# Optimization experiments

Hardware: AMD Instinct MI355X
Metric: run time of the kernel (lower is better)

## Reference

```python
import jax, jax.numpy as jnp
import numpy as np

B, W, K = 8, 200, 100   # batch, window_size, n_features
KS = 7                   # conv kernel size
HID = 150                # GRU hidden dim
ALPHA = 0.2              # leaky relu slope
FE = 2 * W               # feature GAT embed dim (gatv2 doubles window_size)
TE = 2 * K               # temporal GAT embed dim (gatv2 doubles n_features)


def setup_inputs() -> dict:
    key = jax.random.key(0)
    ks = jax.random.split(key, 16)
    s = lambda k, shape, sc=0.05: jax.random.normal(k, shape, jnp.float32) * sc
    return {
        "x": jax.random.normal(ks[0], (B, W, K), jnp.float32),
        "conv_w": s(ks[1], (K, K, KS)),
        "conv_b": s(ks[2], (K,)),
        "f_lin_w": s(ks[3], (2 * W, FE)),
        "f_lin_b": s(ks[4], (FE,)),
        "f_a": s(ks[5], (FE,)),
        "f_bias": s(ks[6], (K, K)),
        "t_lin_w": s(ks[7], (2 * K, TE)),
        "t_lin_b": s(ks[8], (TE,)),
        "t_a": s(ks[9], (TE,)),
        "t_bias": s(ks[10], (W, W)),
        "w_ih": s(ks[11], (3 * HID, 3 * K)),
        "w_hh": s(ks[12], (3 * HID, HID)),
        "b_ih": s(ks[13], (3 * HID,)),
        "b_hh": s(ks[14], (3 * HID,)),
    }


def _leaky(x):
    return jnp.where(x >= 0, x, ALPHA * x)


def _gatv2(v, lin_w, lin_b, a, bias):
    """GATv2 layer over fully-connected graph. v: (b, N, D).
    e_ij = a . leakyrelu(W [v_i || v_j] + b_lin); out = sigmoid(softmax(e+bias) @ v).
    Splitting W rows avoids materializing the (b,N,N,2D) concat tensor."""
    D = v.shape[-1]
    w1, w2 = lin_w[:D], lin_w[D:]
    si = jnp.einsum('bnd,de->bne', v, w1)  # contribution of node i (repeated)
    sj = jnp.einsum('bnd,de->bne', v, w2)  # contribution of node j (alternating)
    g = _leaky(si[:, :, None, :] + sj[:, None, :, :] + lin_b)  # (b,N,N,E)
    e = jnp.einsum('bije,e->bij', g, a) + bias                 # (b,N,N)
    attn = jax.nn.softmax(e, axis=2)
    return jax.nn.sigmoid(jnp.einsum('bij,bjd->bid', attn, v))  # (b,N,D)


def _forward(x, conv_w, conv_b, f_lin_w, f_lin_b, f_a, f_bias,
             t_lin_w, t_lin_b, t_a, t_bias, w_ih, w_hh, b_ih, b_hh):
    # ConvLayer: permute to (b,K,W), pad 3 both sides, conv1d k=7, relu, permute back
    xc = jnp.transpose(x, (0, 2, 1))
    xc = jax.lax.conv_general_dilated(xc, conv_w, (1,), [((KS - 1) // 2, (KS - 1) // 2)],
                                      dimension_numbers=('NCH', 'OIH', 'NCH'))
    xc = jax.nn.relu(xc + conv_b[None, :, None])
    xc = jnp.transpose(xc, (0, 2, 1))  # (b, W, K)

    # Feature GAT: nodes = features, per-node vector = window
    h_feat = _gatv2(jnp.transpose(xc, (0, 2, 1)), f_lin_w, f_lin_b, f_a, f_bias)
    h_feat = jnp.transpose(h_feat, (0, 2, 1))  # (b, W, K)
    # Temporal GAT: nodes = timesteps, per-node vector = features
    h_temp = _gatv2(xc, t_lin_w, t_lin_b, t_a, t_bias)  # (b, W, K)

    h_cat = jnp.concatenate([xc, h_feat, h_temp], axis=2)  # (b, W, 3K)

    # Single-layer GRU, torch gate order (r, z, n), batch_first; return final hidden
    def step(h, xt):
        gi = xt @ w_ih.T + b_ih
        gh = h @ w_hh.T + b_hh
        ir, iz, inn = jnp.split(gi, 3, axis=-1)
        hr, hz, hn = jnp.split(gh, 3, axis=-1)
        r = jax.nn.sigmoid(ir + hr)
        z = jax.nn.sigmoid(iz + hz)
        n = jnp.tanh(inn + r * hn)
        return (1.0 - z) * n + z * h, None

    h0 = jnp.zeros((x.shape[0], HID), x.dtype)
    h_end, _ = jax.lax.scan(step, h0, jnp.transpose(h_cat, (1, 0, 2)))
    return h_end  # (b, HID)


def reference(x, conv_w, conv_b, f_lin_w, f_lin_b, f_a, f_bias,
              t_lin_w, t_lin_b, t_a, t_bias, w_ih, w_hh, b_ih, b_hh):
    return _forward(x, conv_w, conv_b, f_lin_w, f_lin_b, f_a, f_bias,
                    t_lin_w, t_lin_b, t_a, t_bias, w_ih, w_hh, b_ih, b_hh)
```

## Files before the change

### kernel.cpp

```cpp
#include <hip/hip_runtime.h>
#include <math.h>

#define NB   8
#define NW   200
#define NK   100
#define KSZ  7
#define NHID 150
#define NFE  400
#define NTE  200
#define NG   450
#define NCIN 300
#define ALPHAC 0.2f

typedef __attribute__((ext_vector_type(8))) short bf8;
typedef __attribute__((ext_vector_type(4))) float f32x4;

__device__ __forceinline__ float sigmoidf_(float x){
  return 1.0f/(1.0f + __expf(-x));
}
__device__ __forceinline__ float tanhf_(float x){
  float xc = fminf(fmaxf(x, -15.f), 15.f);
  float e = __expf(2.f*xc);
  return (e - 1.f)/(e + 1.f);
}
__device__ __forceinline__ unsigned short f2bf(float f){
  unsigned int u = __float_as_uint(f);
  unsigned int r = u + 0x7FFFu + ((u>>16)&1u);
  return (unsigned short)(r>>16);
}
__device__ __forceinline__ float lrelu_(float x){
  return fmaxf(x, 0.f) + ALPHAC*fminf(x, 0.f);
}

__global__ void prep_kernel(const float* conv_w, const float* w_ih, const float* w_hh,
                            float* conv_wT, float* w_ihT, unsigned int* Bfrag){
  int idx = blockIdx.x*256 + threadIdx.x;
  const int n1 = NK*NK*KSZ;
  const int n2 = NG*NCIN;
  const int n3 = 32*5*64*4;
  if (idx < n1){
    int k = idx % NK; int it = idx / NK;
    int i = it / KSZ, t = it % KSZ;
    conv_wT[idx] = conv_w[(k*NK + i)*KSZ + t];
  } else if (idx < n1 + n2){
    int o = idx - n1; int g = o % NG; int c = o / NG;
    w_ihT[o] = w_ih[g*NCIN + c];
  } else if (idx < n1 + n2 + n3){
    int o = idx - n1 - n2;
    int n   = o / 1280;
    int rem = o % 1280;
    int ks  = rem / 256;
    int rem2= rem % 256;
    int l   = rem2 >> 2;
    int d   = rem2 & 3;
    int col = n*16 + (l & 15);
    int k0  = ks*32 + (l >> 4)*8 + d*2;
    unsigned short lo = 0, hi = 0;
    if (col < NG){
      if (k0     < NHID) lo = f2bf(w_hh[col*NHID + k0]);
      if (k0 + 1 < NHID) hi = f2bf(w_hh[col*NHID + k0 + 1]);
    }
    Bfrag[o] = ((unsigned int)hi << 16) | lo;
  }
}

__global__ void conv_kernel(const float* x, const float* conv_b, const float* conv_wT, float* xc){
  int idx = blockIdx.x*256 + threadIdx.x;
  if (idx >= NB*NW*NK) return;
  int k = idx % NK; int w = (idx/NK) % NW; int b = idx/(NK*NW);
  float acc = conv_b[k];
  const float* xb = x + b*NW*NK;
  for (int t = 0; t < KSZ; ++t){
    int ws = w + t - 3;
    if (ws < 0 || ws >= NW) continue;
    const float* xr = xb + ws*NK;
    const float* wr = conv_wT + t*NK + k;
    #pragma unroll 4
    for (int i = 0; i < NK; ++i){
      acc += xr[i] * wr[i*KSZ*NK];
    }
  }
  xc[idx] = fmaxf(acc, 0.0f);
}

__global__ void fgat_sisj(const float* xc, const float* f_lin_w, float* si, float* sj){
  __shared__ __align__(16) float vt[NW*4];
  int b = blockIdx.x / 25; int n0 = (blockIdx.x % 25)*4;
  int tid = threadIdx.x;
  for (int d = tid; d < NW; d += 512){
    float4 v = *(const float4*)&xc[(b*NW + d)*NK + n0];
    *(float4*)&vt[d*4] = v;
  }
  __syncthreads();
  if (tid >= NFE) return;
  int e = tid;
  float a1[4] = {0,0,0,0}, a2[4] = {0,0,0,0};
  for (int d = 0; d < NW; ++d){
    float w1 = f_lin_w[d*NFE + e];
    float w2 = f_lin_w[(NW + d)*NFE + e];
    float4 v = *(const float4*)&vt[d*4];
    a1[0] += v.x*w1; a1[1] += v.y*w1; a1[2] += v.z*w1; a1[3] += v.w*w1;
    a2[0] += v.x*w2; a2[1] += v.y*w2; a2[2] += v.z*w2; a2[3] += v.w*w2;
  }
  #pragma unroll
  for (int nn = 0; nn < 4; ++nn){
    si[(b*NK + n0+nn)*NFE + e] = a1[nn];
    sj[(b*NK + n0+nn)*NFE + e] = a2[nn];
  }
}

__global__ void tgat_sisj(const float* xc, const float* t_lin_w, float* si, float* sj){
  __shared__ __align__(16) float vt[NK*4];
  int b = blockIdx.x / 50; int n0 = (blockIdx.x % 50)*4;
  int tid = threadIdx.x;
  for (int idx = tid; idx < 4*25; idx += 256){
    int nn = idx & 3; int d4 = idx >> 2;
    float4 v = *(const float4*)&xc[(b*NW + n0+nn)*NK + d4*4];
    vt[(d4*4+0)*4 + nn] = v.x;
    vt[(d4*4+1)*4 + nn] = v.y;
    vt[(d4*4+2)*4 + nn] = v.z;
    vt[(d4*4+3)*4 + nn] = v.w;
  }
  __syncthreads();
  if (tid >= NTE) return;
  int e = tid;
  float a1[4] = {0,0,0,0}, a2[4] = {0,0,0,0};
  for (int d = 0; d < NK; ++d){
    float w1 = t_lin_w[d*NTE + e];
    float w2 = t_lin_w[(NK + d)*NTE + e];
    float4 v = *(const float4*)&vt[d*4];
    a1[0] += v.x*w1; a1[1] += v.y*w1; a1[2] += v.z*w1; a1[3] += v.w*w1;
    a2[0] += v.x*w2; a2[1] += v.y*w2; a2[2] += v.z*w2; a2[3] += v.w*w2;
  }
  #pragma unroll
  for (int nn = 0; nn < 4; ++nn){
    si[(b*NW + n0+nn)*NTE + e] = a1[nn];
    sj[(b*NW + n0+nn)*NTE + e] = a2[nn];
  }
}

__global__ void fgat_attn(const float* xc, const float* si, const float* sj,
                          const float* f_lin_b, const float* f_a, const float* f_bias,
                          float* h_featT){
  __shared__ __align__(16) float sib[NFE];
  __shared__ __align__(16) float av[NFE];
  __shared__ __align__(16) float attn[NK];
  __shared__ float red[128];
  int b = blockIdx.x / NK, i = blockIdx.x % NK;
  int tid = threadIdx.x;
  {
    const float4* si4 = (const float4*)(si + (b*NK + i)*NFE);
    const float4* lb4 = (const float4*)f_lin_b;
    const float4* fa4 = (const float4*)f_a;
    for (int e4 = tid; e4 < NFE/4; e4 += 128){
      float4 s = si4[e4], l = lb4[e4];
      float4 o; o.x=s.x+l.x; o.y=s.y+l.y; o.z=s.z+l.z; o.w=s.w+l.w;
      *(float4*)&sib[e4*4] = o;
      *(float4*)&av[e4*4]  = fa4[e4];
    }
  }
  __syncthreads();
  float ej = -1e30f;
  if (tid < NK){
    const float4* sjr4 = (const float4*)(sj + (b*NK + tid)*NFE);
    const float4* sib4 = (const float4*)sib;
    const float4* av4  = (const float4*)av;
    float acc = 0.f;
    #pragma unroll 4
    for (int e4 = 0; e4 < NFE/4; ++e4){
      float4 s = sjr4[e4], t = sib4[e4], a = av4[e4];
      acc += a.x*lrelu_(t.x+s.x) + a.y*lrelu_(t.y+s.y)
           + a.z*lrelu_(t.z+s.z) + a.w*lrelu_(t.w+s.w);
    }
    ej = acc + f_bias[i*NK + tid];
  }
  red[tid] = ej; __syncthreads();
  for (int s = 64; s > 0; s >>= 1){ if (tid < s) red[tid] = fmaxf(red[tid], red[tid+s]); __syncthreads(); }
  float m = red[0]; __syncthreads();
  float ex = (tid < NK) ? __expf(ej - m) : 0.f;
  red[tid] = ex; __syncthreads();
  for (int s = 64; s > 0; s >>= 1){ if (tid < s) red[tid] += red[tid+s]; __syncthreads(); }
  float denom = red[0];
  if (tid < NK) attn[tid] = ex / denom;
  __syncthreads();
  for (int d = tid; d < NW; d += 128){
    const float4* xr4 = (const float4*)(xc + (b*NW + d)*NK);
    const float4* at4 = (const float4*)attn;
    float acc = 0.f;
    #pragma unroll 5
    for (int j4 = 0; j4 < NK/4; ++j4){
      float4 v = xr4[j4], a = at4[j4];
      acc += a.x*v.x + a.y*v.y + a.z*v.z + a.w*v.w;
    }
    h_featT[(b*NW + d)*NK + i] = sigmoidf_(acc);
  }
}

__global__ void tgat_attn(const float* xc, const float* si, const float* sj,
                          const float* t_lin_b, const float* t_a, const float* t_bias,
                          float* h_temp){
  __shared__ __align__(16) float sib[NTE];
  __shared__ __align__(16) float av[NTE];
  __shared__ __align__(16) float attn[NW];
  __shared__ float red[256];
  int b = blockIdx.x / NW, i = blockIdx.x % NW;
  int tid = threadIdx.x;
  {
    const float4* si4 = (const float4*)(si + (b*NW + i)*NTE);
    const float4* lb4 = (const float4*)t_lin_b;
    const float4* ta4 = (const float4*)t_a;
    for (int e4 = tid; e4 < NTE/4; e4 += 256){
      float4 s = si4[e4], l = lb4[e4];
      float4 o; o.x=s.x+l.x; o.y=s.y+l.y; o.z=s.z+l.z; o.w=s.w+l.w;
      *(float4*)&sib[e4*4] = o;
      *(float4*)&av[e4*4]  = ta4[e4];
    }
  }
  __syncthreads();
  float ej = -1e30f;
  if (tid < NW){
    const float4* sjr4 = (const float4*)(sj + (b*NW + tid)*NTE);
    const float4* sib4 = (const float4*)sib;
    const float4* av4  = (const float4*)av;
    float acc = 0.f;
    #pragma unroll 4
    for (int e4 = 0; e4 < NTE/4; ++e4){
      float4 s = sjr4[e4], t = sib4[e4], a = av4[e4];
      acc += a.x*lrelu_(t.x+s.x) + a.y*lrelu_(t.y+s.y)
           + a.z*lrelu_(t.z+s.z) + a.w*lrelu_(t.w+s.w);
    }
    ej = acc + t_bias[i*NW + tid];
  }
  red[tid] = ej; __syncthreads();
  for (int s = 128; s > 0; s >>= 1){ if (tid < s) red[tid] = fmaxf(red[tid], red[tid+s]); __syncthreads(); }
  float m = red[0]; __syncthreads();
  float ex = (tid < NW) ? __expf(ej - m) : 0.f;
  red[tid] = ex; __syncthreads();
  for (int s = 128; s > 0; s >>= 1){ if (tid < s) red[tid] += red[tid+s]; __syncthreads(); }
  float denom = red[0];
  if (tid < NW) attn[tid] = ex / denom;
  __syncthreads();
  for (int d = tid; d < NK; d += 256){
    float acc = 0.f;
    #pragma unroll 4
    for (int j = 0; j < NW; ++j) acc += attn[j]*xc[(b*NW + j)*NK + d];
    h_temp[(b*NW + i)*NK + d] = sigmoidf_(acc);
  }
}

__global__ void gi_kernel(const float* xc, const float* h_featT, const float* h_temp,
                          const float* w_ihT, const float* b_ih, float* gi){
  __shared__ __align__(16) float hc[NCIN*8];
  int b = blockIdx.x / 25; int t0 = (blockIdx.x % 25)*8;
  int tid = threadIdx.x;
  for (int idx = tid; idx < NCIN*8; idx += 512){
    int tt = idx / NCIN; int c = idx % NCIN;
    int base = (b*NW + t0 + tt)*NK;
    float v;
    if (c < NK)        v = xc[base + c];
    else if (c < 2*NK) v = h_featT[base + c - NK];
    else               v = h_temp[base + c - 2*NK];
    hc[c*8 + tt] = v;
  }
  __syncthreads();
  if (tid >= NG) return;
  int g = tid;
  float bi = b_ih[g];
  float acc[8];
  #pragma unroll
  for (int tt = 0; tt < 8; ++tt) acc[tt] = bi;
  for (int c = 0; c < NCIN; ++c){
    float wv = w_ihT[c*NG + g];
    float4 h0 = *(const float4*)&hc[c*8];
    float4 h1 = *(const float4*)&hc[c*8+4];
    acc[0] += h0.x*wv; acc[1] += h0.y*wv; acc[2] += h0.z*wv; acc[3] += h0.w*wv;
    acc[4] += h1.x*wv; acc[5] += h1.y*wv; acc[6] += h1.z*wv; acc[7] += h1.w*wv;
  }
  #pragma unroll
  for (int tt = 0; tt < 8; ++tt)
    gi[((t0+tt)*NB + b)*NG + g] = acc[tt];
}

#define STASH(B0,B1,B2,B3, FR) { \
  int4 wq = Bq[(FR)*64 + lane]; \
  asm volatile("v_accvgpr_write_b32 " B0 ", %0\n\t" \
               "v_accvgpr_write_b32 " B1 ", %1\n\t" \
               "v_accvgpr_write_b32 " B2 ", %2\n\t" \
               "v_accvgpr_write_b32 " B3 ", %3" \
               :: "v"(wq.x), "v"(wq.y), "v"(wq.z), "v"(wq.w) \
               : B0, B1, B2, B3); }
#define MMA_INIT(ACC, AF, BR, C0,C1,C2,C3) \
  asm volatile("v_mfma_f32_16x16x32_bf16 %0, %1, " BR ", 0" \
               : "=v"(ACC) : "v"(AF) : C0,C1,C2,C3);
#define MMA_ACC(ACC, AF, BR, C0,C1,C2,C3) \
  asm volatile("v_mfma_f32_16x16x32_bf16 %0, %1, " BR ", %0" \
               : "+v"(ACC) : "v"(AF) : C0,C1,C2,C3);

__global__ void __launch_bounds__(768) gru_kernel(const float* gi, const int4* Bq,
                                                  const float* b_hh, float* out){
  __shared__ __align__(16) unsigned short h_bf[16*184];
  __shared__ __align__(16) float gh[512*10];
  int tid = threadIdx.x;
  int lane = tid & 63;
  int wv = tid >> 6;
  int agrp = lane >> 4;
  int arow = lane & 15;

  int b0 = tid/NHID, u0 = tid%NHID;
  bool v1 = (tid < 432);
  int p1 = tid + 768;
  int b1 = v1 ? p1/NHID : 0, u1 = v1 ? p1%NHID : 0;
  float bhr0 = b_hh[u0], bhz0 = b_hh[NHID+u0], bhn0 = b_hh[2*NHID+u0];
  float bhr1 = b_hh[u1], bhz1 = b_hh[NHID+u1], bhn1 = b_hh[2*NHID+u1];

  if (wv < 8){
    STASH("a0","a1","a2","a3",     (wv)*5+0)
    STASH("a4","a5","a6","a7",     (wv)*5+1)
    STASH("a8","a9","a10","a11",   (wv)*5+2)
    STASH("a12","a13","a14","a15", (wv)*5+3)
    STASH("a16","a17","a18","a19", (wv)*5+4)
    STASH("a20","a21","a22","a23", (wv+8)*5+0)
    STASH("a24","a25","a26","a27", (wv+8)*5+1)
    STASH("a28","a29","a30","a31", (wv+8)*5+2)
    STASH("a32","a33","a34","a35", (wv+8)*5+3)
    STASH("a36","a37","a38","a39", (wv+8)*5+4)
    STASH("a40","a41","a42","a43", (wv+16)*5+0)
    STASH("a44","a45","a46","a47", (wv+16)*5+1)
    STASH("a48","a49","a50","a51", (wv+16)*5+2)
    STASH("a52","a53","a54","a55", (wv+16)*5+3)
    STASH("a56","a57","a58","a59", (wv+16)*5+4)
    STASH("a60","a61","a62","a63", (wv+24)*5+0)
    STASH("a64","a65","a66","a67", (wv+24)*5+1)
    STASH("a68","a69","a70","a71", (wv+24)*5+2)
    STASH("a72","a73","a74","a75", (wv+24)*5+3)
    STASH("a76","a77","a78","a79", (wv+24)*5+4)
  }

  for (int i = tid; i < 16*184; i += 768) h_bf[i] = 0;
  __syncthreads();

  const bf8* HB = (const bf8*)h_bf;
  int abase = arow*23 + agrp;

  float hold0 = 0.f, hold1 = 0.f;

  float cr0, cz0, cn0, cr1 = 0.f, cz1 = 0.f, cn1 = 0.f;
  {
    const float* g0 = gi + b0*NG;
    cr0 = g0[u0]; cz0 = g0[NHID+u0]; cn0 = g0[2*NHID+u0];
    if (v1){
      const float* g1 = gi + b1*NG;
      cr1 = g1[u1]; cz1 = g1[NHID+u1]; cn1 = g1[2*NHID+u1];
    }
  }

  for (int t = 0; t < NW; ++t){
    int tn = (t+1 < NW) ? (t+1) : t;
    const float* gt = gi + tn*NB*NG;
    float nr0 = gt[b0*NG+u0], nz0 = gt[b0*NG+NHID+u0], nn0 = gt[b0*NG+2*NHID+u0];
    float nr1 = 0.f, nz1 = 0.f, nn1 = 0.f;
    if (v1){ nr1 = gt[b1*NG+u1]; nz1 = gt[b1*NG+NHID+u1]; nn1 = gt[b1*NG+2*NHID+u1]; }

    if (wv < 8){
      bf8 A0 = HB[abase],    A1 = HB[abase+4],  A2 = HB[abase+8],
          A3 = HB[abase+12], A4 = HB[abase+16];
      f32x4 c0, c1, c2, c3;
      MMA_INIT(c0, A0, "a[0:3]",   "a0","a1","a2","a3")
      MMA_INIT(c1, A0, "a[20:23]", "a20","a21","a22","a23")
      MMA_INIT(c2, A0, "a[40:43]", "a40","a41","a42","a43")
      MMA_INIT(c3, A0, "a[60:63]", "a60","a61","a62","a63")
      MMA_ACC (c0, A1, "a[4:7]",   "a4","a5","a6","a7")
      MMA_ACC (c1, A1, "a[24:27]", "a24","a25","a26","a27")
      MMA_ACC (c2, A1, "a[44:47]", "a44","a45","a46","a47")
      MMA_ACC (c3, A1, "a[64:67]", "a64","a65","a66","a67")
      MMA_ACC (c0, A2, "a[8:11]",  "a8","a9","a10","a11")
      MMA_ACC (c1, A2, "a[28:31]", "a28","a29","a30","a31")
      MMA_ACC (c2, A2, "a[48:51]", "a48","a49","a50","a51")
      MMA_ACC (c3, A2, "a[68:71]", "a68","a69","a70","a71")
      MMA_ACC (c0, A3, "a[12:15]", "a12","a13","a14","a15")
      MMA_ACC (c1, A3, "a[32:35]", "a32","a33","a34","a35")
      MMA_ACC (c2, A3, "a[52:55]", "a52","a53","a54","a55")
      MMA_ACC (c3, A3, "a[72:75]", "a72","a73","a74","a75")
      MMA_ACC (c0, A4, "a[16:19]", "a16","a17","a18","a19")
      MMA_ACC (c1, A4, "a[36:39]", "a36","a37","a38","a39")
      MMA_ACC (c2, A4, "a[56:59]", "a56","a57","a58","a59")
      MMA_ACC (c3, A4, "a[76:79]", "a76","a77","a78","a79")
      asm volatile("s_nop 7\n\ts_nop 7" ::: );

      int cb = agrp*2;
      float2 s0, s1, s2, s3;
      s0.x = c0[0]+c0[1]; s0.y = c0[2]+c0[3];
      s1.x = c1[0]+c1[1]; s1.y = c1[2]+c1[3];
      s2.x = c2[0]+c2[1]; s2.y = c2[2]+c2[3];
      s3.x = c3[0]+c3[1]; s3.y = c3[2]+c3[3];
      *(float2*)&gh[((wv    )*16 + arow)*10 + cb] = s0;
      *(float2*)&gh[((wv+ 8)*16 + arow)*10 + cb] = s1;
      *(float2*)&gh[((wv+16)*16 + arow)*10 + cb] = s2;
      *(float2*)&gh[((wv+24)*16 + arow)*10 + cb] = s3;
    }
    __syncthreads();

    {
      float r = sigmoidf_(cr0 + gh[u0*10 + b0]        + bhr0);
      float z = sigmoidf_(cz0 + gh[(NHID+u0)*10 + b0] + bhz0);
      float n = tanhf_  (cn0 + r*(gh[(2*NHID+u0)*10 + b0] + bhn0));
      float hn = (1.f - z)*n + z*hold0;
      hold0 = hn;
      unsigned int ub = __float_as_uint(hn);
      unsigned int hi = (ub + 0x7FFFu + ((ub>>16)&1u)) >> 16;
      h_bf[(2*b0)*184 + u0] = (unsigned short)hi;
      float lo = hn - __uint_as_float(hi<<16);
      unsigned int ul = __float_as_uint(lo);
      h_bf[(2*b0+1)*184 + u0] = (unsigned short)((ul + 0x7FFFu + ((ul>>16)&1u)) >> 16);
    }
    if (v1){
      float r = sigmoidf_(cr1 + gh[u1*10 + b1]        + bhr1);
      float z = sigmoidf_(cz1 + gh[(NHID+u1)*10 + b1] + bhz1);
      float n = tanhf_  (cn1 + r*(gh[(2*NHID+u1)*10 + b1] + bhn1));
      float hn = (1.f - z)*n + z*hold1;
      hold1 = hn;
      unsigned int ub = __float_as_uint(hn);
      unsigned int hi = (ub + 0x7FFFu + ((ub>>16)&1u)) >> 16;
      h_bf[(2*b1)*184 + u1] = (unsigned short)hi;
      float lo = hn - __uint_as_float(hi<<16);
      unsigned int ul = __float_as_uint(lo);
      h_bf[(2*b1+1)*184 + u1] = (unsigned short)((ul + 0x7FFFu + ((ul>>16)&1u)) >> 16);
    }
    __syncthreads();

    cr0 = nr0; cz0 = nz0; cn0 = nn0;
    cr1 = nr1; cz1 = nz1; cn1 = nn1;
  }

  out[b0*NHID + u0] = hold0;
  if (v1) out[b1*NHID + u1] = hold1;
}

extern "C" void kernel_launch(void* const* d_in, const int* in_sizes, int n_in,
                              void* d_out, int out_size, void* d_ws, size_t ws_size,
                              hipStream_t stream){
  const float* x       = (const float*)d_in[0];
  const float* conv_w  = (const float*)d_in[1];
  const float* conv_b  = (const float*)d_in[2];
  const float* f_lin_w = (const float*)d_in[3];
  const float* f_lin_b = (const float*)d_in[4];
  const float* f_a     = (const float*)d_in[5];
  const float* f_bias  = (const float*)d_in[6];
  const float* t_lin_w = (const float*)d_in[7];
  const float* t_lin_b = (const float*)d_in[8];
  const float* t_a     = (const float*)d_in[9];
  const float* t_bias  = (const float*)d_in[10];
  const float* w_ih    = (const float*)d_in[11];
  const float* w_hh    = (const float*)d_in[12];
  const float* b_ih    = (const float*)d_in[13];
  const float* b_hh    = (const float*)d_in[14];

  float* ws      = (float*)d_ws;
  float* xc      = ws;
  float* conv_wT = ws + 160000;
  float* si_f    = ws + 230000;
  float* sj_f    = ws + 550000;
  float* h_featT = ws + 870000;
  float* si_t    = ws + 1030000;
  float* sj_t    = ws + 1350000;
  float* h_temp  = ws + 1670000;
  float* w_ihT   = ws + 1830000;
  float* gi      = ws + 1965000;
  float* BfragF  = ws + 2685000;

  prep_kernel<<<961, 256, 0, stream>>>(conv_w, w_ih, w_hh, conv_wT, w_ihT, (unsigned int*)BfragF);
  conv_kernel<<<(NB*NW*NK + 255)/256, 256, 0, stream>>>(x, conv_b, conv_wT, xc);
  fgat_sisj<<<NB*25, 512, 0, stream>>>(xc, f_lin_w, si_f, sj_f);
  tgat_sisj<<<NB*50, 256, 0, stream>>>(xc, t_lin_w, si_t, sj_t);
  fgat_attn<<<NB*NK, 128, 0, stream>>>(xc, si_f, sj_f, f_lin_b, f_a, f_bias, h_featT);
  tgat_attn<<<NB*NW, 256, 0, stream>>>(xc, si_t, sj_t, t_lin_b, t_a, t_bias, h_temp);
  gi_kernel<<<NB*25, 512, 0, stream>>>(xc, h_featT, h_temp, w_ihT, b_ih, gi);
  gru_kernel<<<1, 768, 0, stream>>>(gi, (const int4*)BfragF, b_hh, (float*)d_out);
}
```

Before: 402.8 us.

## Merge GAT kernels, use wave-shuffle softmax, fold GRU biases, use packed bf16 convert

The feature and temporal si/sj projection kernels are merged into one launch that branches on block index, and the two attention kernels are merged the same way. Both attention paths now use 256 threads with wave-level shuffle reductions in place of shared-memory tree reductions. The r and z parts of b_hh are folded into gi so the GRU loop skips those adds. The per-step bf16 hi/lo split now uses the v_cvt_pk_bf16_f32 instruction, and the loop walks precomputed pointers. These changes aim to cut launch overhead, barriers and per-step work on the serial GRU path. The cost is longer branchy kernels and a last-step prefetch that reads one step past the end of gi.

Result: no change. 398.9 us (-0.9%).

```diff
diff --git a/kernel.cpp b/kernel.cpp
--- a/kernel.cpp
+++ b/kernel.cpp
@@ -83,173 +83,182 @@
   xc[idx] = fmaxf(acc, 0.0f);
 }
 
-__global__ void fgat_sisj(const float* xc, const float* f_lin_w, float* si, float* sj){
+__global__ void sisj_fused(const float* xc, const float* f_lin_w, float* si_f, float* sj_f,
+                           const float* t_lin_w, float* si_t, float* sj_t){
   __shared__ __align__(16) float vt[NW*4];
-  int b = blockIdx.x / 25; int n0 = (blockIdx.x % 25)*4;
   int tid = threadIdx.x;
-  for (int d = tid; d < NW; d += 512){
-    float4 v = *(const float4*)&xc[(b*NW + d)*NK + n0];
-    *(float4*)&vt[d*4] = v;
-  }
-  __syncthreads();
-  if (tid >= NFE) return;
-  int e = tid;
-  float a1[4] = {0,0,0,0}, a2[4] = {0,0,0,0};
-  for (int d = 0; d < NW; ++d){
-    float w1 = f_lin_w[d*NFE + e];
-    float w2 = f_lin_w[(NW + d)*NFE + e];
-    float4 v = *(const float4*)&vt[d*4];
-    a1[0] += v.x*w1; a1[1] += v.y*w1; a1[2] += v.z*w1; a1[3] += v.w*w1;
-    a2[0] += v.x*w2; a2[1] += v.y*w2; a2[2] += v.z*w2; a2[3] += v.w*w2;
-  }
-  #pragma unroll
-  for (int nn = 0; nn < 4; ++nn){
-    si[(b*NK + n0+nn)*NFE + e] = a1[nn];
-    sj[(b*NK + n0+nn)*NFE + e] = a2[nn];
-  }
-}
-
-__global__ void tgat_sisj(const float* xc, const float* t_lin_w, float* si, float* sj){
-  __shared__ __align__(16) float vt[NK*4];
-  int b = blockIdx.x / 50; int n0 = (blockIdx.x % 50)*4;
-  int tid = threadIdx.x;
-  for (int idx = tid; idx < 4*25; idx += 256){
-    int nn = idx & 3; int d4 = idx >> 2;
-    float4 v = *(const float4*)&xc[(b*NW + n0+nn)*NK + d4*4];
-    vt[(d4*4+0)*4 + nn] = v.x;
-    vt[(d4*4+1)*4 + nn] = v.y;
-    vt[(d4*4+2)*4 + nn] = v.z;
-    vt[(d4*4+3)*4 + nn] = v.w;
-  }
-  __syncthreads();
-  if (tid >= NTE) return;
-  int e = tid;
-  float a1[4] = {0,0,0,0}, a2[4] = {0,0,0,0};
-  for (int d = 0; d < NK; ++d){
-    float w1 = t_lin_w[d*NTE + e];
-    float w2 = t_lin_w[(NK + d)*NTE + e];
-    float4 v = *(const float4*)&vt[d*4];
-    a1[0] += v.x*w1; a1[1] += v.y*w1; a1[2] += v.z*w1; a1[3] += v.w*w1;
-    a2[0] += v.x*w2; a2[1] += v.y*w2; a2[2] += v.z*w2; a2[3] += v.w*w2;
-  }
-  #pragma unroll
-  for (int nn = 0; nn < 4; ++nn){
-    si[(b*NW + n0+nn)*NTE + e] = a1[nn];
-    sj[(b*NW + n0+nn)*NTE + e] = a2[nn];
-  }
-}
-
-__global__ void fgat_attn(const float* xc, const float* si, const float* sj,
-                          const float* f_lin_b, const float* f_a, const float* f_bias,
-                          float* h_featT){
+  if (blockIdx.x < 200){
+    int b = blockIdx.x / 25; int n0 = (blockIdx.x % 25)*4;
+    for (int d = tid; d < NW; d += 512){
+      float4 v = *(const float4*)&xc[(b*NW + d)*NK + n0];
+      *(float4*)&vt[d*4] = v;
+    }
+    __syncthreads();
+    if (tid >= NFE) return;
+    int e = tid;
+    float a1[4] = {0,0,0,0}, a2[4] = {0,0,0,0};
+    for (int d = 0; d < NW; ++d){
+      float w1 = f_lin_w[d*NFE + e];
+      float w2 = f_lin_w[(NW + d)*NFE + e];
+      float4 v = *(const float4*)&vt[d*4];
+      a1[0] += v.x*w1; a1[1] += v.y*w1; a1[2] += v.z*w1; a1[3] += v.w*w1;
+      a2[0] += v.x*w2; a2[1] += v.y*w2; a2[2] += v.z*w2; a2[3] += v.w*w2;
+    }
+    #pragma unroll
+    for (int nn = 0; nn < 4; ++nn){
+      si_f[(b*NK + n0+nn)*NFE + e] = a1[nn];
+      sj_f[(b*NK + n0+nn)*NFE + e] = a2[nn];
+    }
+  } else {
+    int bi = blockIdx.x - 200;
+    int b = bi / 50; int n0 = (bi % 50)*4;
+    for (int idx = tid; idx < 4*25; idx += 512){
+      int nn = idx & 3; int d4 = idx >> 2;
+      float4 v = *(const float4*)&xc[(b*NW + n0+nn)*NK + d4*4];
+      vt[(d4*4+0)*4 + nn] = v.x;
+      vt[(d4*4+1)*4 + nn] = v.y;
+      vt[(d4*4+2)*4 + nn] = v.z;
+      vt[(d4*4+3)*4 + nn] = v.w;
+    }
+    __syncthreads();
+    if (tid >= NTE) return;
+    int e = tid;
+    float a1[4] = {0,0,0,0}, a2[4] = {0,0,0,0};
+    for (int d = 0; d < NK; ++d){
+      float w1 = t_lin_w[d*NTE + e];
+      float w2 = t_lin_w[(NK + d)*NTE + e];
+      float4 v = *(const float4*)&vt[d*4];
+      a1[0] += v.x*w1; a1[1] += v.y*w1; a1[2] += v.z*w1; a1[3] += v.w*w1;
+      a2[0] += v.x*w2; a2[1] += v.y*w2; a2[2] += v.z*w2; a2[3] += v.w*w2;
+    }
+    #pragma unroll
+    for (int nn = 0; nn < 4; ++nn){
+      si_t[(b*NW + n0+nn)*NTE + e] = a1[nn];
+      sj_t[(b*NW + n0+nn)*NTE + e] = a2[nn];
+    }
+  }
+}
+
+__global__ void attn_fused(const float* xc,
+                           const float* si_f, const float* sj_f, const float* f_lin_b,
+                           const float* f_a, const float* f_bias,
+                           const float* si_t, const float* sj_t, const float* t_lin_b,
+                           const float* t_a, const float* t_bias,
+                           float* h_featT, float* h_temp){
   __shared__ __align__(16) float sib[NFE];
   __shared__ __align__(16) float av[NFE];
-  __shared__ __align__(16) float attn[NK];
-  __shared__ float red[128];
-  int b = blockIdx.x / NK, i = blockIdx.x % NK;
-  int tid = threadIdx.x;
-  {
-    const float4* si4 = (const float4*)(si + (b*NK + i)*NFE);
-    const float4* lb4 = (const float4*)f_lin_b;
-    const float4* fa4 = (const float4*)f_a;
-    for (int e4 = tid; e4 < NFE/4; e4 += 128){
-      float4 s = si4[e4], l = lb4[e4];
-      float4 o; o.x=s.x+l.x; o.y=s.y+l.y; o.z=s.z+l.z; o.w=s.w+l.w;
-      *(float4*)&sib[e4*4] = o;
-      *(float4*)&av[e4*4]  = fa4[e4];
-    }
-  }
-  __syncthreads();
-  float ej = -1e30f;
-  if (tid < NK){
-    const float4* sjr4 = (const float4*)(sj + (b*NK + tid)*NFE);
-    const float4* sib4 = (const float4*)sib;
-    const float4* av4  = (const float4*)av;
-    float acc = 0.f;
-    #pragma unroll 4
-    for (int e4 = 0; e4 < NFE/4; ++e4){
-      float4 s = sjr4[e4], t = sib4[e4], a = av4[e4];
-      acc += a.x*lrelu_(t.x+s.x) + a.y*lrelu_(t.y+s.y)
-           + a.z*lrelu_(t.z+s.z) + a.w*lrelu_(t.w+s.w);
-    }
-    ej = acc + f_bias[i*NK + tid];
-  }
-  red[tid] = ej; __syncthreads();
-  for (int s = 64; s > 0; s >>= 1){ if (tid < s) red[tid] = fmaxf(red[tid], red[tid+s]); __syncthreads(); }
-  float m = red[0]; __syncthreads();
-  float ex = (tid < NK) ? __expf(ej - m) : 0.f;
-  red[tid] = ex; __syncthreads();
-  for (int s = 64; s > 0; s >>= 1){ if (tid < s) red[tid] += red[tid+s]; __syncthreads(); }
-  float denom = red[0];
-  if (tid < NK) attn[tid] = ex / denom;
-  __syncthreads();
-  for (int d = tid; d < NW; d += 128){
-    const float4* xr4 = (const float4*)(xc + (b*NW + d)*NK);
-    const float4* at4 = (const float4*)attn;
-    float acc = 0.f;
-    #pragma unroll 5
-    for (int j4 = 0; j4 < NK/4; ++j4){
-      float4 v = xr4[j4], a = at4[j4];
-      acc += a.x*v.x + a.y*v.y + a.z*v.z + a.w*v.w;
-    }
-    h_featT[(b*NW + d)*NK + i] = sigmoidf_(acc);
-  }
-}
-
-__global__ void tgat_attn(const float* xc, const float* si, const float* sj,
-                          const float* t_lin_b, const float* t_a, const float* t_bias,
-                          float* h_temp){
-  __shared__ __align__(16) float sib[NTE];
-  __shared__ __align__(16) float av[NTE];
   __shared__ __align__(16) float attn[NW];
-  __shared__ float red[256];
-  int b = blockIdx.x / NW, i = blockIdx.x % NW;
-  int tid = threadIdx.x;
-  {
-    const float4* si4 = (const float4*)(si + (b*NW + i)*NTE);
-    const float4* lb4 = (const float4*)t_lin_b;
-    const float4* ta4 = (const float4*)t_a;
-    for (int e4 = tid; e4 < NTE/4; e4 += 256){
-      float4 s = si4[e4], l = lb4[e4];
-      float4 o; o.x=s.x+l.x; o.y=s.y+l.y; o.z=s.z+l.z; o.w=s.w+l.w;
-      *(float4*)&sib[e4*4] = o;
-      *(float4*)&av[e4*4]  = ta4[e4];
-    }
-  }
-  __syncthreads();
-  float ej = -1e30f;
-  if (tid < NW){
-    const float4* sjr4 = (const float4*)(sj + (b*NW + tid)*NTE);
-    const float4* sib4 = (const float4*)sib;
-    const float4* av4  = (const float4*)av;
-    float acc = 0.f;
-    #pragma unroll 4
-    for (int e4 = 0; e4 < NTE/4; ++e4){
-      float4 s = sjr4[e4], t = sib4[e4], a = av4[e4];
-      acc += a.x*lrelu_(t.x+s.x) + a.y*lrelu_(t.y+s.y)
-           + a.z*lrelu_(t.z+s.z) + a.w*lrelu_(t.w+s.w);
-    }
-    ej = acc + t_bias[i*NW + tid];
-  }
-  red[tid] = ej; __syncthreads();
-  for (int s = 128; s > 0; s >>= 1){ if (tid < s) red[tid] = fmaxf(red[tid], red[tid+s]); __syncthreads(); }
-  float m = red[0]; __syncthreads();
-  float ex = (tid < NW) ? __expf(ej - m) : 0.f;
-  red[tid] = ex; __syncthreads();
-  for (int s = 128; s > 0; s >>= 1){ if (tid < s) red[tid] += red[tid+s]; __syncthreads(); }
-  float denom = red[0];
-  if (tid < NW) attn[tid] = ex / denom;
-  __syncthreads();
-  for (int d = tid; d < NK; d += 256){
-    float acc = 0.f;
-    #pragma unroll 4
-    for (int j = 0; j < NW; ++j) acc += attn[j]*xc[(b*NW + j)*NK + d];
-    h_temp[(b*NW + i)*NK + d] = sigmoidf_(acc);
+  __shared__ float red[8];
+  int tid = threadIdx.x, lane = tid & 63, wid = tid >> 6;
+  if (blockIdx.x < NB*NK){
+    int b = blockIdx.x / NK, i = blockIdx.x % NK;
+    {
+      const float4* si4 = (const float4*)(si_f + (b*NK + i)*NFE);
+      const float4* lb4 = (const float4*)f_lin_b;
+      const float4* fa4 = (const float4*)f_a;
+      for (int e4 = tid; e4 < NFE/4; e4 += 256){
+        float4 s = si4[e4], l = lb4[e4];
+        float4 o; o.x=s.x+l.x; o.y=s.y+l.y; o.z=s.z+l.z; o.w=s.w+l.w;
+        *(float4*)&sib[e4*4] = o;
+        *(float4*)&av[e4*4]  = fa4[e4];
+      }
+    }
+    __syncthreads();
+    float ej = -1e30f;
+    if (tid < NK){
+      const float4* sjr4 = (const float4*)(sj_f + (b*NK + tid)*NFE);
+      const float4* sib4 = (const float4*)sib;
+      const float4* av4  = (const float4*)av;
+      float acc = 0.f;
+      #pragma unroll 4
+      for (int e4 = 0; e4 < NFE/4; ++e4){
+        float4 s = sjr4[e4], t = sib4[e4], a = av4[e4];
+        acc += a.x*lrelu_(t.x+s.x) + a.y*lrelu_(t.y+s.y)
+             + a.z*lrelu_(t.z+s.z) + a.w*lrelu_(t.w+s.w);
+      }
+      ej = acc + f_bias[i*NK + tid];
+    }
+    float m = ej;
+    #pragma unroll
+    for (int off = 32; off > 0; off >>= 1) m = fmaxf(m, __shfl_xor(m, off));
+    if (lane == 0) red[wid] = m;
+    __syncthreads();
+    float bm = fmaxf(fmaxf(red[0], red[1]), fmaxf(red[2], red[3]));
+    float ex = (tid < NK) ? __expf(ej - bm) : 0.f;
+    float s = ex;
+    #pragma unroll
+    for (int off = 32; off > 0; off >>= 1) s += __shfl_xor(s, off);
+    if (lane == 0) red[4 + wid] = s;
+    __syncthreads();
+    float denom = red[4] + red[5] + red[6] + red[7];
+    if (tid < NK) attn[tid] = ex / denom;
+    __syncthreads();
+    for (int d = tid; d < NW; d += 256){
+      const float4* xr4 = (const float4*)(xc + (b*NW + d)*NK);
+      const float4* at4 = (const float4*)attn;
+      float acc = 0.f;
+      #pragma unroll 5
+      for (int j4 = 0; j4 < NK/4; ++j4){
+        float4 v = xr4[j4], a = at4[j4];
+        acc += a.x*v.x + a.y*v.y + a.z*v.z + a.w*v.w;
+      }
+      h_featT[(b*NW + d)*NK + i] = sigmoidf_(acc);
+    }
+  } else {
+    int bi = blockIdx.x - NB*NK;
+    int b = bi / NW, i = bi % NW;
+    {
+      const float4* si4 = (const float4*)(si_t + (b*NW + i)*NTE);
+      const float4* lb4 = (const float4*)t_lin_b;
+      const float4* ta4 = (const float4*)t_a;
+      for (int e4 = tid; e4 < NTE/4; e4 += 256){
+        float4 s = si4[e4], l = lb4[e4];
+        float4 o; o.x=s.x+l.x; o.y=s.y+l.y; o.z=s.z+l.z; o.w=s.w+l.w;
+        *(float4*)&sib[e4*4] = o;
+        *(float4*)&av[e4*4]  = ta4[e4];
+      }
+    }
+    __syncthreads();
+    float ej = -1e30f;
+    if (tid < NW){
+      const float4* sjr4 = (const float4*)(sj_t + (b*NW + tid)*NTE);
+      const float4* sib4 = (const float4*)sib;
+      const float4* av4  = (const float4*)av;
+      float acc = 0.f;
+      #pragma unroll 4
+      for (int e4 = 0; e4 < NTE/4; ++e4){
+        float4 s = sjr4[e4], t = sib4[e4], a = av4[e4];
+        acc += a.x*lrelu_(t.x+s.x) + a.y*lrelu_(t.y+s.y)
+             + a.z*lrelu_(t.z+s.z) + a.w*lrelu_(t.w+s.w);
+      }
+      ej = acc + t_bias[i*NW + tid];
+    }
+    float m = ej;
+    #pragma unroll
+    for (int off = 32; off > 0; off >>= 1) m = fmaxf(m, __shfl_xor(m, off));
+    if (lane == 0) red[wid] = m;
+    __syncthreads();
+    float bm = fmaxf(fmaxf(red[0], red[1]), fmaxf(red[2], red[3]));
+    float ex = (tid < NW) ? __expf(ej - bm) : 0.f;
+    float s = ex;
+    #pragma unroll
+    for (int off = 32; off > 0; off >>= 1) s += __shfl_xor(s, off);
+    if (lane == 0) red[4 + wid] = s;
+    __syncthreads();
+    float denom = red[4] + red[5] + red[6] + red[7];
+    if (tid < NW) attn[tid] = ex / denom;
+    __syncthreads();
+    for (int d = tid; d < NK; d += 256){
+      float acc = 0.f;
+      #pragma unroll 4
+      for (int j = 0; j < NW; ++j) acc += attn[j]*xc[(b*NW + j)*NK + d];
+      h_temp[(b*NW + i)*NK + d] = sigmoidf_(acc);
+    }
   }
 }
 
 __global__ void gi_kernel(const float* xc, const float* h_featT, const float* h_temp,
-                          const float* w_ihT, const float* b_ih, float* gi){
+                          const float* w_ihT, const float* b_ih, const float* b_hh, float* gi){
   __shared__ __align__(16) float hc[NCIN*8];
   int b = blockIdx.x / 25; int t0 = (blockIdx.x % 25)*8;
   int tid = threadIdx.x;
@@ -265,7 +274,7 @@
   __syncthreads();
   if (tid >= NG) return;
   int g = tid;
-  float bi = b_ih[g];
+  float bi = b_ih[g] + ((g < 2*NHID) ? b_hh[g] : 0.f);
   float acc[8];
   #pragma unroll
   for (int tt = 0; tt < 8; ++tt) acc[tt] = bi;
@@ -296,6 +305,13 @@
   asm volatile("v_mfma_f32_16x16x32_bf16 %0, %1, " BR ", %0" \
                : "+v"(ACC) : "v"(AF) : C0,C1,C2,C3);
 
+__device__ __forceinline__ void pack_hilo(float hn, unsigned int& hi2, unsigned int& lo2){
+  asm("v_cvt_pk_bf16_f32 %0, %1, %1" : "=v"(hi2) : "v"(hn));
+  float hif = __uint_as_float(hi2 << 16);
+  float lo = hn - hif;
+  asm("v_cvt_pk_bf16_f32 %0, %1, %1" : "=v"(lo2) : "v"(lo));
+}
+
 __global__ void __launch_bounds__(768) gru_kernel(const float* gi, const int4* Bq,
                                                   const float* b_hh, float* out){
   __shared__ __align__(16) unsigned short h_bf[16*184];
@@ -310,8 +326,8 @@
   bool v1 = (tid < 432);
   int p1 = tid + 768;
   int b1 = v1 ? p1/NHID : 0, u1 = v1 ? p1%NHID : 0;
-  float bhr0 = b_hh[u0], bhz0 = b_hh[NHID+u0], bhn0 = b_hh[2*NHID+u0];
-  float bhr1 = b_hh[u1], bhz1 = b_hh[NHID+u1], bhn1 = b_hh[2*NHID+u1];
+  float bhn0 = b_hh[2*NHID+u0];
+  float bhn1 = b_hh[2*NHID+u1];
 
   if (wv < 8){
     STASH("a0","a1","a2","a3",     (wv)*5+0)
@@ -344,22 +360,24 @@
 
   float hold0 = 0.f, hold1 = 0.f;
 
-  float cr0, cz0, cn0, cr1 = 0.f, cz1 = 0.f, cn1 = 0.f;
-  {
-    const float* g0 = gi + b0*NG;
-    cr0 = g0[u0]; cz0 = g0[NHID+u0]; cn0 = g0[2*NHID+u0];
-    if (v1){
-      const float* g1 = gi + b1*NG;
-      cr1 = g1[u1]; cz1 = g1[NHID+u1]; cn1 = g1[2*NHID+u1];
-    }
-  }
+  const float* gp0 = gi + b0*NG + u0;
+  const float* gp1 = gi + b1*NG + u1;
+  float cr0 = gp0[0], cz0 = gp0[NHID], cn0 = gp0[2*NHID];
+  float cr1 = 0.f, cz1 = 0.f, cn1 = 0.f;
+  if (v1){ cr1 = gp1[0]; cz1 = gp1[NHID]; cn1 = gp1[2*NHID]; }
+
+  const float* ghp0 = &gh[u0*10 + b0];
+  const float* ghp1 = &gh[u1*10 + b1];
+  unsigned short* hb0h = &h_bf[(2*b0)*184 + u0];
+  unsigned short* hb0l = &h_bf[(2*b0+1)*184 + u0];
+  unsigned short* hb1h = &h_bf[(2*b1)*184 + u1];
+  unsigned short* hb1l = &h_bf[(2*b1+1)*184 + u1];
 
   for (int t = 0; t < NW; ++t){
-    int tn = (t+1 < NW) ? (t+1) : t;
-    const float* gt = gi + tn*NB*NG;
-    float nr0 = gt[b0*NG+u0], nz0 = gt[b0*NG+NHID+u0], nn0 = gt[b0*NG+2*NHID+u0];
+    gp0 += NB*NG; gp1 += NB*NG;
+    float nr0 = gp0[0], nz0 = gp0[NHID], nn0 = gp0[2*NHID];
     float nr1 = 0.f, nz1 = 0.f, nn1 = 0.f;
-    if (v1){ nr1 = gt[b1*NG+u1]; nz1 = gt[b1*NG+NHID+u1]; nn1 = gt[b1*NG+2*NHID+u1]; }
+    if (v1){ nr1 = gp1[0]; nz1 = gp1[NHID]; nn1 = gp1[2*NHID]; }
 
     if (wv < 8){
       bf8 A0 = HB[abase],    A1 = HB[abase+4],  A2 = HB[abase+8],
@@ -401,30 +419,26 @@
     __syncthreads();
 
     {
-      float r = sigmoidf_(cr0 + gh[u0*10 + b0]        + bhr0);
-      float z = sigmoidf_(cz0 + gh[(NHID+u0)*10 + b0] + bhz0);
-      float n = tanhf_  (cn0 + r*(gh[(2*NHID+u0)*10 + b0] + bhn0));
+      float r = sigmoidf_(cr0 + ghp0[0]);
+      float z = sigmoidf_(cz0 + ghp0[NHID*10]);
+      float n = tanhf_  (cn0 + r*(ghp0[2*NHID*10] + bhn0));
       float hn = (1.f - z)*n + z*hold0;
       hold0 = hn;
-      unsigned int ub = __float_as_uint(hn);
-      unsigned int hi = (ub + 0x7FFFu + ((ub>>16)&1u)) >> 16;
-      h_bf[(2*b0)*184 + u0] = (unsigned short)hi;
-      float lo = hn - __uint_as_float(hi<<16);
-      unsigned int ul = __float_as_uint(lo);
-      h_bf[(2*b0+1)*184 + u0] = (unsigned short)((ul + 0x7FFFu + ((ul>>16)&1u)) >> 16);
+      unsigned int hi2, lo2;
+      pack_hilo(hn, hi2, lo2);
+      *hb0h = (unsigned short)hi2;
+      *hb0l = (unsigned short)lo2;
     }
     if (v1){
-      float r = sigmoidf_(cr1 + gh[u1*10 + b1]        + bhr1);
-      float z = sigmoidf_(cz1 + gh[(NHID+u1)*10 + b1] + bhz1);
-      float n = tanhf_  (cn1 + r*(gh[(2*NHID+u1)*10 + b1] + bhn1));
+      float r = sigmoidf_(cr1 + ghp1[0]);
+      float z = sigmoidf_(cz1 + ghp1[NHID*10]);
+      float n = tanhf_  (cn1 + r*(ghp1[2*NHID*10] + bhn1));
       float hn = (1.f - z)*n + z*hold1;
       hold1 = hn;
-      unsigned int ub = __float_as_uint(hn);
-      unsigned int hi = (ub + 0x7FFFu + ((ub>>16)&1u)) >> 16;
-      h_bf[(2*b1)*184 + u1] = (unsigned short)hi;
-      float lo = hn - __uint_as_float(hi<<16);
-      unsigned int ul = __float_as_uint(lo);
-      h_bf[(2*b1+1)*184 + u1] = (unsigned short)((ul + 0x7FFFu + ((ul>>16)&1u)) >> 16);
+      unsigned int hi2, lo2;
+      pack_hilo(hn, hi2, lo2);
+      *hb1h = (unsigned short)hi2;
+      *hb1l = (unsigned short)lo2;
     }
     __syncthreads();
 
@@ -470,10 +484,9 @@
 
   prep_kernel<<<961, 256, 0, stream>>>(conv_w, w_ih, w_hh, conv_wT, w_ihT, (unsigned int*)BfragF);
   conv_kernel<<<(NB*NW*NK + 255)/256, 256, 0, stream>>>(x, conv_b, conv_wT, xc);
-  fgat_sisj<<<NB*25, 512, 0, stream>>>(xc, f_lin_w, si_f, sj_f);
-  tgat_sisj<<<NB*50, 256, 0, stream>>>(xc, t_lin_w, si_t, sj_t);
-  fgat_attn<<<NB*NK, 128, 0, stream>>>(xc, si_f, sj_f, f_lin_b, f_a, f_bias, h_featT);
-  tgat_attn<<<NB*NW, 256, 0, stream>>>(xc, si_t, sj_t, t_lin_b, t_a, t_bias, h_temp);
-  gi_kernel<<<NB*25, 512, 0, stream>>>(xc, h_featT, h_temp, w_ihT, b_ih, gi);
+  sisj_fused<<<600, 512, 0, stream>>>(xc, f_lin_w, si_f, sj_f, t_lin_w, si_t, sj_t);
+  attn_fused<<<2400, 256, 0, stream>>>(xc, si_f, sj_f, f_lin_b, f_a, f_bias,
+                                       si_t, sj_t, t_lin_b, t_a, t_bias, h_featT, h_temp);
+  gi_kernel<<<200, 512, 0, stream>>>(xc, h_featT, h_temp, w_ihT, b_ih, b_hh, gi);
   gru_kernel<<<1, 768, 0, stream>>>(gi, (const int4*)BfragF, b_hh, (float*)d_out);
 }
```
